# Performance work log

Hardware: AMD Instinct MI355X
Metric: run time of the kernel (lower is better)

## Reference

```python
import jax, jax.numpy as jnp
import numpy as np

B, N, D = 16, 4096, 128
M = 2048  # codebook size
EPS = 1e-10


def setup_inputs() -> dict:
    key = jax.random.key(0)
    kx, kw = jax.random.split(key)
    x = jax.random.normal(kx, (B, N, D), dtype=jnp.float32)
    # codebook (nn.Embedding weight, kaiming-uniform init ~ uniform(-bound, bound))
    bound = np.sqrt(6.0 / D)
    weight = jax.random.uniform(kw, (M, D), dtype=jnp.float32, minval=-bound, maxval=bound)
    return {"x": x, "weight": weight}


def reference(x, weight):
    b, n, d = x.shape
    m = weight.shape[0]
    q = x.reshape(b * n, d)                       # (bn, d)
    # squared L2 distances: ||q||^2 + ||k||^2 - 2 q.k  (temperature==0 -> argmax of -dist)
    l2_q = jnp.sum(q * q, axis=1, keepdims=True)  # (bn, 1)
    l2_k = jnp.sum(weight * weight, axis=1)       # (m,)
    sim = q @ weight.T                            # (bn, m)  GEMM
    dist = l2_q + l2_k - 2.0 * sim
    indices = jnp.argmin(dist, axis=1)            # (bn,)
    z = weight[indices]                           # onehot @ k == gather
    quantized = z.reshape(b, n, d)
    # straight-through estimator (training path): q + (z - q).detach()
    quantized_st = x + jax.lax.stop_gradient(quantized - x)
    # commitment loss: mse(quantized.detach(), x)
    loss = jnp.mean((jax.lax.stop_gradient(quantized_st) - x) ** 2)
    # perplexity over codebook usage (h == 1 head)
    counts = jnp.zeros((m,), dtype=x.dtype).at[indices].add(1.0)
    p = counts / (b * n)                          # mean of onehot over (b, n)
    perp = jnp.exp(-jnp.sum(p * jnp.log(p + EPS)))[None]  # shape (1,) == 'h'
    out_indices = indices.reshape(b, 1, n)
    return quantized_st, loss, perp, out_indices
```

## Files before the change

### kernel.cpp

```cpp
#include <hip/hip_runtime.h>
#include <hip/hip_bf16.h>
#include <math.h>

#define D_DIM 128
#define M_CODES 2048
#define BN_TOT 65536
#define OUT_LOSS 8388608
#define OUT_PERP 8388609
#define OUT_IDX 8388610
#define MARGIN 2e-3f

#define QB 128

#define WS_L2K 0
#define WS_PB 8192
#define WS_IDX 1056768
#define WS_PART 1318912
#define WS_CNT 1351680
#define WS_FLAGCNT 1359872
#define WS_FLAGGED 1360896

typedef __bf16 bf16x8 __attribute__((ext_vector_type(8)));
typedef float f32x4 __attribute__((ext_vector_type(4)));

#define GLOAD_LDS16(g, l)                                         \
  __builtin_amdgcn_global_load_lds(                               \
      (const __attribute__((address_space(1))) void*)(g),         \
      (__attribute__((address_space(3))) void*)(l), 16, 0, 0)

#define MFMA16(a, b, c) __builtin_amdgcn_mfma_f32_16x16x32_bf16((a), (b), (c), 0, 0, 0)

__global__ __launch_bounds__(256) void prep_kernel(const float* __restrict__ w,
                                                   float* __restrict__ l2k,
                                                   __bf16* __restrict__ pb,
                                                   int* __restrict__ counts,
                                                   int* __restrict__ flagcnt) {
  int gid = blockIdx.x * 256 + threadIdx.x;

  if (gid < M_CODES) {
    const float4* p = (const float4*)(w + (size_t)gid * D_DIM);
    double s = 0.0;
#pragma unroll
    for (int j = 0; j < 32; ++j) {
      float4 v = p[j];
      s += (double)(v.x * v.x);
      s += (double)(v.y * v.y);
      s += (double)(v.z * v.z);
      s += (double)(v.w * v.w);
    }
    l2k[gid] = (float)s;
    counts[gid] = 0;
    if (gid == 0) *flagcnt = 0;
  }

  int lane = gid & 63;
  int g = gid >> 6;
  int cid = g & 15;
  int p = g >> 4;
  int k2 = cid & 7;
  int ks = k2 >> 1;
  int wc = k2 & 1;
  int code = p * 32 + wc * 16 + (lane & 15);
  int koff = ks * 32 + (lane >> 4) * 8;
  const float* src = w + (size_t)code * D_DIM + koff;
  float4 u = *(const float4*)src;
  float4 v = *(const float4*)(src + 4);
  float f[8] = {u.x, u.y, u.z, u.w, v.x, v.y, v.z, v.w};
  bf16x8 o;
#pragma unroll
  for (int j = 0; j < 8; ++j) {
    __bf16 hh = (__bf16)f[j];
    o[j] = (cid < 8) ? hh : (__bf16)(f[j] - (float)hh);
  }
  *(bf16x8*)(pb + (size_t)g * 512 + lane * 8) = o;
}

__device__ __forceinline__ void merge_bs(float& b, float& s, int& i,
                                         float ob, float os, int oi) {
  if (ob > b) {
    s = fmaxf(b, os);
    b = ob;
    i = oi;
  } else if (ob < b) {
    s = fmaxf(s, ob);
  } else {
    s = b;
    if (oi < i) i = oi;
  }
}

__global__ __launch_bounds__(512, 4) void argmin_mfma(
    const float* __restrict__ x, const __bf16* __restrict__ pb,
    const float* __restrict__ l2k, int* __restrict__ best_idx,
    int* __restrict__ flag_count, int* __restrict__ flagged) {
  __shared__ __align__(16) unsigned char ldsB[2 * 32768];
  __shared__ float redB[8][32];
  __shared__ float redS[8][32];
  __shared__ int redI[8][32];

  const int tid = threadIdx.x;
  const int wv = tid >> 6;
  const int lane = tid & 63;
  const int col = lane & 15;
  const int quad = lane >> 4;
  const int wc = wv & 1;
  const int wq = wv >> 1;
  const int q0 = blockIdx.x * QB;

  bf16x8 ah[2][4], al[2][4];
#pragma unroll
  for (int mt = 0; mt < 2; ++mt) {
#pragma unroll
    for (int ks = 0; ks < 4; ++ks) {
      const float* xr =
          x + (size_t)(q0 + wq * 32 + 16 * mt + col) * D_DIM + 32 * ks + 8 * quad;
      float4 u = *(const float4*)xr;
      float4 v = *(const float4*)(xr + 4);
      float f[8] = {u.x, u.y, u.z, u.w, v.x, v.y, v.z, v.w};
      bf16x8 h, l;
#pragma unroll
      for (int j = 0; j < 8; ++j) {
        __bf16 hh = (__bf16)f[j];
        h[j] = hh;
        l[j] = (__bf16)(f[j] - (float)hh);
      }
      ah[mt][ks] = h;
      al[mt][ks] = l;
    }
  }

  float m1[2][4], m2[2][4];
  int bp[2][4];
#pragma unroll
  for (int mt = 0; mt < 2; ++mt)
#pragma unroll
    for (int r = 0; r < 4; ++r) {
      m1[mt][r] = -3.4e38f;
      m2[mt][r] = -3.4e38f;
      bp[mt][r] = 0;
    }

  const int ldsw = wc * 1024 + lane * 16;
  const float* l2p = l2k + wc * 16 + col;

  auto stage = [&](int ch, unsigned char* db) {
    const char* s = (const char*)pb + (size_t)ch * 32768 + wv * 4096 + lane * 16;
#pragma unroll
    for (int i = 0; i < 4; ++i) GLOAD_LDS16(s + i * 1024, db + i * 1024);
  };

  stage(0, ldsB + wv * 4096);
  float l2a = l2p[0];
  float l2b = l2p[32];
  __syncthreads();

#pragma unroll 1
  for (int ch = 0; ch < 32; ++ch) {
    const int buf = ch & 1;
    if (ch < 31) stage(ch + 1, ldsB + (buf ^ 1) * 32768 + wv * 4096);
    float l2na = 0.f, l2nb = 0.f;
    if (ch < 31) {
      l2na = l2p[(2 * ch + 2) * 32];
      l2nb = l2p[(2 * ch + 3) * 32];
    }

    const unsigned char* rb = ldsB + buf * 32768 + ldsw;
    float ia = -0.5f * l2a, ib = -0.5f * l2b;
    f32x4 a00 = (f32x4){ia, ia, ia, ia};
    f32x4 a10 = (f32x4){ia, ia, ia, ia};
    f32x4 a01 = (f32x4){ib, ib, ib, ib};
    f32x4 a11 = (f32x4){ib, ib, ib, ib};

    bf16x8 h0 = *(const bf16x8*)(rb);
    bf16x8 l0 = *(const bf16x8*)(rb + 8192);
    bf16x8 h1 = *(const bf16x8*)(rb + 16384);
    bf16x8 l1 = *(const bf16x8*)(rb + 24576);

#define DO_KS(KS, PRE)                                                    \
    {                                                                     \
      bf16x8 nh0, nl0, nh1, nl1;                                          \
      if (PRE) {                                                          \
        nh0 = *(const bf16x8*)(rb + ((KS) + 1) * 2048);                   \
        nl0 = *(const bf16x8*)(rb + 8192 + ((KS) + 1) * 2048);            \
        nh1 = *(const bf16x8*)(rb + 16384 + ((KS) + 1) * 2048);           \
        nl1 = *(const bf16x8*)(rb + 24576 + ((KS) + 1) * 2048);           \
      }                                                                   \
      a00 = MFMA16(al[0][KS], h0, a00);                                   \
      a10 = MFMA16(al[1][KS], h0, a10);                                   \
      a01 = MFMA16(al[0][KS], h1, a01);                                   \
      a11 = MFMA16(al[1][KS], h1, a11);                                   \
      a00 = MFMA16(ah[0][KS], l0, a00);                                   \
      a10 = MFMA16(ah[1][KS], l0, a10);                                   \
      a01 = MFMA16(ah[0][KS], l1, a01);                                   \
      a11 = MFMA16(ah[1][KS], l1, a11);                                   \
      a00 = MFMA16(ah[0][KS], h0, a00);                                   \
      a10 = MFMA16(ah[1][KS], h0, a10);                                   \
      a01 = MFMA16(ah[0][KS], h1, a01);                                   \
      a11 = MFMA16(ah[1][KS], h1, a11);                                   \
      if (PRE) { h0 = nh0; l0 = nl0; h1 = nh1; l1 = nl1; }                \
    }
    DO_KS(0, 1)
    DO_KS(1, 1)
    DO_KS(2, 1)
    DO_KS(3, 0)
#undef DO_KS

#pragma unroll
    for (int mt = 0; mt < 2; ++mt) {
#pragma unroll
      for (int r = 0; r < 4; ++r) {
        float dd = (mt == 0) ? a00[r] : a10[r];
        bool gt = dd > m1[mt][r];
        m2[mt][r] = fmaxf(m2[mt][r], fminf(m1[mt][r], dd));
        bp[mt][r] = gt ? (ch * 2 + 0) : bp[mt][r];
        m1[mt][r] = fmaxf(m1[mt][r], dd);
      }
    }
#pragma unroll
    for (int mt = 0; mt < 2; ++mt) {
#pragma unroll
      for (int r = 0; r < 4; ++r) {
        float dd = (mt == 0) ? a01[r] : a11[r];
        bool gt = dd > m1[mt][r];
        m2[mt][r] = fmaxf(m2[mt][r], fminf(m1[mt][r], dd));
        bp[mt][r] = gt ? (ch * 2 + 1) : bp[mt][r];
        m1[mt][r] = fmaxf(m1[mt][r], dd);
      }
    }

    l2a = l2na;
    l2b = l2nb;
    __syncthreads();
  }

#pragma unroll
  for (int mt = 0; mt < 2; ++mt) {
#pragma unroll
    for (int r = 0; r < 4; ++r) {
      float b = m1[mt][r], s = m2[mt][r];
      int i = bp[mt][r] * 32 + wc * 16 + col;
#pragma unroll
      for (int m = 1; m < 16; m <<= 1) {
        float ob = __shfl_xor(b, m);
        float os = __shfl_xor(s, m);
        int oi = __shfl_xor(i, m);
        merge_bs(b, s, i, ob, os, oi);
      }
      if (col == 0) {
        int qloc = 16 * mt + 4 * quad + r;
        redB[wv][qloc] = b;
        redS[wv][qloc] = s;
        redI[wv][qloc] = i;
      }
    }
  }
  __syncthreads();

  if (tid < QB) {
    int wg = tid >> 5;
    int ql = tid & 31;
    float b = -3.4e38f, s = -3.4e38f;
    int i = 0x7fffffff;
    merge_bs(b, s, i, redB[wg * 2 + 0][ql], redS[wg * 2 + 0][ql], redI[wg * 2 + 0][ql]);
    merge_bs(b, s, i, redB[wg * 2 + 1][ql], redS[wg * 2 + 1][ql], redI[wg * 2 + 1][ql]);
    best_idx[q0 + tid] = i;
    if (2.0f * (b - s) < MARGIN) {
      int pos = atomicAdd(flag_count, 1);
      flagged[pos] = q0 + tid;
    }
  }
}

__global__ __launch_bounds__(256) void fixup_kernel(const float* __restrict__ x,
                                                    const float* __restrict__ w,
                                                    const float* __restrict__ l2k32,
                                                    const int* __restrict__ flagged,
                                                    const int* __restrict__ flag_count,
                                                    int* __restrict__ best_idx) {
  __shared__ float qs[D_DIM];
  __shared__ float l2q_sh;
  __shared__ float redD[256];
  __shared__ int redI[256];
  const int tid = threadIdx.x;
  const int n = *flag_count;
  for (int f = blockIdx.x; f < n; f += gridDim.x) {
    __syncthreads();
    int q = flagged[f];
    if (tid < D_DIM) qs[tid] = x[(size_t)q * D_DIM + tid];
    __syncthreads();
    if (tid == 0) {
      double s = 0.0;
      for (int d = 0; d < D_DIM; ++d) {
        float t = qs[d] * qs[d];
        s += (double)t;
      }
      l2q_sh = (float)s;
    }
    __syncthreads();
    const float l2q = l2q_sh;
    float bd = 3.4e38f;
    int bi = 0x7fffffff;
    for (int c = tid; c < M_CODES; c += 256) {
      const float4* wr = (const float4*)(w + (size_t)c * D_DIM);
      double s = 0.0;
#pragma unroll
      for (int j = 0; j < 32; ++j) {
        float4 v = wr[j];
        s = fma((double)qs[j * 4 + 0], (double)v.x, s);
        s = fma((double)qs[j * 4 + 1], (double)v.y, s);
        s = fma((double)qs[j * 4 + 2], (double)v.z, s);
        s = fma((double)qs[j * 4 + 3], (double)v.w, s);
      }
      float simf = (float)s;
      float S = l2q + l2k32[c];
      float T = 2.0f * simf;
      float dist = S - T;
      if (dist < bd) { bd = dist; bi = c; }
    }
    redD[tid] = bd;
    redI[tid] = bi;
    __syncthreads();
    for (int off = 128; off; off >>= 1) {
      if (tid < off) {
        float od = redD[tid + off];
        int oi = redI[tid + off];
        if (od < redD[tid] || (od == redD[tid] && oi < redI[tid])) {
          redD[tid] = od;
          redI[tid] = oi;
        }
      }
      __syncthreads();
    }
    if (tid == 0) best_idx[q] = redI[0];
  }
}

__global__ __launch_bounds__(256) void epilogue_kernel(const float* __restrict__ x,
                                                       const float* __restrict__ w,
                                                       const int* __restrict__ best_idx,
                                                       float* __restrict__ out,
                                                       float* __restrict__ part,
                                                       int* __restrict__ counts) {
  int gid = blockIdx.x * 256 + threadIdx.x;
  int q = gid >> 5;
  int d4 = gid & 31;
  int idx = best_idx[q];
  float4 xv = ((const float4*)x)[gid];
  float4 wv = ((const float4*)w)[(size_t)idx * 32 + d4];
  float4 o;
  float t0 = wv.x - xv.x; o.x = xv.x + t0; float e0 = o.x - xv.x;
  float t1 = wv.y - xv.y; o.y = xv.y + t1; float e1 = o.y - xv.y;
  float t2 = wv.z - xv.z; o.z = xv.z + t2; float e2 = o.z - xv.z;
  float t3 = wv.w - xv.w; o.w = xv.w + t3; float e3 = o.w - xv.w;
  float ls = e0 * e0 + e1 * e1 + e2 * e2 + e3 * e3;
  ((float4*)out)[gid] = o;

  for (int off = 32; off; off >>= 1) ls += __shfl_down(ls, off);
  __shared__ float red[4];
  if ((threadIdx.x & 63) == 0) red[threadIdx.x >> 6] = ls;
  __syncthreads();
  if (threadIdx.x == 0) part[blockIdx.x] = red[0] + red[1] + red[2] + red[3];

  if (d4 == 0) {
    out[OUT_IDX + q] = (float)idx;
    atomicAdd(&counts[idx], 1);
  }
}

__global__ __launch_bounds__(256) void finalize_kernel(const int* __restrict__ counts,
                                                       const float* __restrict__ part,
                                                       float* __restrict__ out) {
  int tid = threadIdx.x;
  float ls = 0.f;
  for (int i = tid; i < 8192; i += 256) ls += part[i];
  float es = 0.f;
  for (int i = tid; i < M_CODES; i += 256) {
    float p = (float)counts[i] * (1.0f / 65536.0f);
    es += p * logf(p + 1e-10f);
  }
  for (int off = 32; off; off >>= 1) {
    ls += __shfl_down(ls, off);
    es += __shfl_down(es, off);
  }
  __shared__ float redl[4], rede[4];
  if ((tid & 63) == 0) {
    redl[tid >> 6] = ls;
    rede[tid >> 6] = es;
  }
  __syncthreads();
  if (tid == 0) {
    out[OUT_LOSS] = (redl[0] + redl[1] + redl[2] + redl[3]) * (1.0f / 8388608.0f);
    out[OUT_PERP] = expf(-(rede[0] + rede[1] + rede[2] + rede[3]));
  }
}

extern "C" void kernel_launch(void* const* d_in, const int* in_sizes, int n_in,
                              void* d_out, int out_size, void* d_ws, size_t ws_size,
                              hipStream_t stream) {
  const float* x = (const float*)d_in[0];
  const float* w = (const float*)d_in[1];
  float* out = (float*)d_out;
  char* ws = (char*)d_ws;
  float* l2k = (float*)(ws + WS_L2K);
  __bf16* pb = (__bf16*)(ws + WS_PB);
  int* bidx = (int*)(ws + WS_IDX);
  float* part = (float*)(ws + WS_PART);
  int* counts = (int*)(ws + WS_CNT);
  int* flagcnt = (int*)(ws + WS_FLAGCNT);
  int* flagged = (int*)(ws + WS_FLAGGED);

  prep_kernel<<<256, 256, 0, stream>>>(w, l2k, pb, counts, flagcnt);
  argmin_mfma<<<BN_TOT / QB, 512, 0, stream>>>(x, pb, l2k, bidx, flagcnt, flagged);
  fixup_kernel<<<256, 256, 0, stream>>>(x, w, l2k, flagged, flagcnt, bidx);
  epilogue_kernel<<<8192, 256, 0, stream>>>(x, w, bidx, out, part, counts);
  finalize_kernel<<<1, 256, 0, stream>>>(counts, part, out);
}
```

Before: 238.1 us.

## Fuse straight-through epilogue into argmin kernel and flagged-row fixup

Removes the separate epilogue kernel. The argmin kernel now writes quantized outputs, indices, counts and per-block loss partials for every unflagged row it finishes, reusing x rows that are likely still in cache. The fixup kernel handles the epilogue for flagged rows and accumulates their loss through an atomic into an extra partial slot; its grid also grows from 256 to 1024 blocks. This saves one launch and a second full pass over x, at the cost of a longer argmin tail and a float atomic whose summation order is not deterministic.

Measured after the change: 229.6 us. -3.6%, faster.

```diff
diff --git a/kernel.cpp b/kernel.cpp
--- a/kernel.cpp
+++ b/kernel.cpp
@@ -34,7 +34,8 @@
                                                    float* __restrict__ l2k,
                                                    __bf16* __restrict__ pb,
                                                    int* __restrict__ counts,
-                                                   int* __restrict__ flagcnt) {
+                                                   int* __restrict__ flagcnt,
+                                                   float* __restrict__ part) {
   int gid = blockIdx.x * 256 + threadIdx.x;
 
   if (gid < M_CODES) {
@@ -51,6 +52,7 @@
     l2k[gid] = (float)s;
     counts[gid] = 0;
     if (gid == 0) *flagcnt = 0;
+    if (gid == 1) part[512] = 0.f;
   }
 
   int lane = gid & 63;
@@ -91,12 +93,17 @@
 
 __global__ __launch_bounds__(512, 4) void argmin_mfma(
     const float* __restrict__ x, const __bf16* __restrict__ pb,
-    const float* __restrict__ l2k, int* __restrict__ best_idx,
-    int* __restrict__ flag_count, int* __restrict__ flagged) {
+    const float* __restrict__ l2k, const float* __restrict__ w,
+    float* __restrict__ out, int* __restrict__ best_idx,
+    int* __restrict__ flag_count, int* __restrict__ flagged,
+    float* __restrict__ part, int* __restrict__ counts) {
   __shared__ __align__(16) unsigned char ldsB[2 * 32768];
   __shared__ float redB[8][32];
   __shared__ float redS[8][32];
   __shared__ int redI[8][32];
+  __shared__ int flagmask[QB];
+  __shared__ int bidx_sh[QB];
+  __shared__ float lred[8];
 
   const int tid = threadIdx.x;
   const int wv = tid >> 6;
@@ -264,10 +271,46 @@
     merge_bs(b, s, i, redB[wg * 2 + 0][ql], redS[wg * 2 + 0][ql], redI[wg * 2 + 0][ql]);
     merge_bs(b, s, i, redB[wg * 2 + 1][ql], redS[wg * 2 + 1][ql], redI[wg * 2 + 1][ql]);
     best_idx[q0 + tid] = i;
-    if (2.0f * (b - s) < MARGIN) {
+    bidx_sh[tid] = i;
+    int fl = (2.0f * (b - s) < MARGIN) ? 1 : 0;
+    flagmask[tid] = fl;
+    if (fl) {
       int pos = atomicAdd(flag_count, 1);
       flagged[pos] = q0 + tid;
-    }
+    } else {
+      out[OUT_IDX + q0 + tid] = (float)i;
+      atomicAdd(&counts[i], 1);
+    }
+  }
+  __syncthreads();
+
+  const float4* x4 = (const float4*)x;
+  const float4* w4 = (const float4*)w;
+  float4* o4 = (float4*)out;
+  float ls = 0.f;
+  for (int f4 = tid; f4 < QB * 32; f4 += 512) {
+    int ql = f4 >> 5;
+    int d4 = f4 & 31;
+    if (!flagmask[ql]) {
+      size_t gi = (size_t)(q0 + ql) * 32 + d4;
+      float4 xv = x4[gi];
+      float4 wvv = w4[(size_t)bidx_sh[ql] * 32 + d4];
+      float4 o;
+      float t0 = wvv.x - xv.x; o.x = xv.x + t0; float e0 = o.x - xv.x;
+      float t1 = wvv.y - xv.y; o.y = xv.y + t1; float e1 = o.y - xv.y;
+      float t2 = wvv.z - xv.z; o.z = xv.z + t2; float e2 = o.z - xv.z;
+      float t3 = wvv.w - xv.w; o.w = xv.w + t3; float e3 = o.w - xv.w;
+      ls += e0 * e0 + e1 * e1 + e2 * e2 + e3 * e3;
+      o4[gi] = o;
+    }
+  }
+  for (int off = 32; off; off >>= 1) ls += __shfl_down(ls, off);
+  if (lane == 0) lred[wv] = ls;
+  __syncthreads();
+  if (tid == 0) {
+    float t = 0.f;
+    for (int i = 0; i < 8; ++i) t += lred[i];
+    part[blockIdx.x] = t;
   }
 }
 
@@ -276,7 +319,10 @@
                                                     const float* __restrict__ l2k32,
                                                     const int* __restrict__ flagged,
                                                     const int* __restrict__ flag_count,
-                                                    int* __restrict__ best_idx) {
+                                                    int* __restrict__ best_idx,
+                                                    float* __restrict__ out,
+                                                    float* __restrict__ part,
+                                                    int* __restrict__ counts) {
   __shared__ float qs[D_DIM];
   __shared__ float l2q_sh;
   __shared__ float redD[256];
@@ -331,39 +377,27 @@
       }
       __syncthreads();
     }
-    if (tid == 0) best_idx[q] = redI[0];
-  }
-}
-
-__global__ __launch_bounds__(256) void epilogue_kernel(const float* __restrict__ x,
-                                                       const float* __restrict__ w,
-                                                       const int* __restrict__ best_idx,
-                                                       float* __restrict__ out,
-                                                       float* __restrict__ part,
-                                                       int* __restrict__ counts) {
-  int gid = blockIdx.x * 256 + threadIdx.x;
-  int q = gid >> 5;
-  int d4 = gid & 31;
-  int idx = best_idx[q];
-  float4 xv = ((const float4*)x)[gid];
-  float4 wv = ((const float4*)w)[(size_t)idx * 32 + d4];
-  float4 o;
-  float t0 = wv.x - xv.x; o.x = xv.x + t0; float e0 = o.x - xv.x;
-  float t1 = wv.y - xv.y; o.y = xv.y + t1; float e1 = o.y - xv.y;
-  float t2 = wv.z - xv.z; o.z = xv.z + t2; float e2 = o.z - xv.z;
-  float t3 = wv.w - xv.w; o.w = xv.w + t3; float e3 = o.w - xv.w;
-  float ls = e0 * e0 + e1 * e1 + e2 * e2 + e3 * e3;
-  ((float4*)out)[gid] = o;
-
-  for (int off = 32; off; off >>= 1) ls += __shfl_down(ls, off);
-  __shared__ float red[4];
-  if ((threadIdx.x & 63) == 0) red[threadIdx.x >> 6] = ls;
-  __syncthreads();
-  if (threadIdx.x == 0) part[blockIdx.x] = red[0] + red[1] + red[2] + red[3];
-
-  if (d4 == 0) {
-    out[OUT_IDX + q] = (float)idx;
-    atomicAdd(&counts[idx], 1);
+    const int idx = redI[0];
+    if (tid == 0) {
+      best_idx[q] = idx;
+      out[OUT_IDX + q] = (float)idx;
+      atomicAdd(&counts[idx], 1);
+    }
+    float lsq = 0.f;
+    if (tid < 32) {
+      size_t gi = (size_t)q * 32 + tid;
+      float4 xv = ((const float4*)x)[gi];
+      float4 wvv = ((const float4*)w)[(size_t)idx * 32 + tid];
+      float4 o;
+      float t0 = wvv.x - xv.x; o.x = xv.x + t0; float e0 = o.x - xv.x;
+      float t1 = wvv.y - xv.y; o.y = xv.y + t1; float e1 = o.y - xv.y;
+      float t2 = wvv.z - xv.z; o.z = xv.z + t2; float e2 = o.z - xv.z;
+      float t3 = wvv.w - xv.w; o.w = xv.w + t3; float e3 = o.w - xv.w;
+      lsq = e0 * e0 + e1 * e1 + e2 * e2 + e3 * e3;
+      ((float4*)out)[gi] = o;
+    }
+    for (int off = 32; off; off >>= 1) lsq += __shfl_down(lsq, off);
+    if (tid == 0) atomicAdd(&part[512], lsq);
   }
 }
 
@@ -372,7 +406,7 @@
                                                        float* __restrict__ out) {
   int tid = threadIdx.x;
   float ls = 0.f;
-  for (int i = tid; i < 8192; i += 256) ls += part[i];
+  for (int i = tid; i < 513; i += 256) ls += part[i];
   float es = 0.f;
   for (int i = tid; i < M_CODES; i += 256) {
     float p = (float)counts[i] * (1.0f / 65536.0f);
@@ -409,9 +443,10 @@
   int* flagcnt = (int*)(ws + WS_FLAGCNT);
   int* flagged = (int*)(ws + WS_FLAGGED);
 
-  prep_kernel<<<256, 256, 0, stream>>>(w, l2k, pb, counts, flagcnt);
-  argmin_mfma<<<BN_TOT / QB, 512, 0, stream>>>(x, pb, l2k, bidx, flagcnt, flagged);
-  fixup_kernel<<<256, 256, 0, stream>>>(x, w, l2k, flagged, flagcnt, bidx);
-  epilogue_kernel<<<8192, 256, 0, stream>>>(x, w, bidx, out, part, counts);
+  prep_kernel<<<256, 256, 0, stream>>>(w, l2k, pb, counts, flagcnt, part);
+  argmin_mfma<<<BN_TOT / QB, 512, 0, stream>>>(x, pb, l2k, w, out, bidx,
+                                               flagcnt, flagged, part, counts);
+  fixup_kernel<<<1024, 256, 0, stream>>>(x, w, l2k, flagged, flagcnt, bidx,
+                                         out, part, counts);
   finalize_kernel<<<1, 256, 0, stream>>>(counts, part, out);
 }
```
